# Kernel tuning notes

Hardware: AMD Instinct MI355X
Metric: run time of the kernel (lower is better)

The kernel has to match this reference:

```python
import jax, jax.numpy as jnp
import numpy as np

EPSILON = 1e-8
NUM_STEPS = 1000
S_OFFSET = 0.0001
POWER = 2
CLIPMAX = 0.999
B = 1048576


def _schedule():
    t = jnp.arange(0, NUM_STEPS + 1, dtype=jnp.float32)
    f_t = jnp.cos(np.pi / 2 * (t / NUM_STEPS + S_OFFSET) / (1 + S_OFFSET)) ** POWER
    alpha_bars = f_t / f_t[0]
    betas = jnp.concatenate([jnp.zeros([1], jnp.float32), 1.0 - alpha_bars[1:] / alpha_bars[:-1]])
    betas = jnp.minimum(betas, CLIPMAX)
    sigmas = jnp.sqrt(betas[1:] * ((1.0 - alpha_bars[:-1]) / (1.0 - alpha_bars[1:])))
    sigmas = jnp.concatenate([jnp.zeros([1], jnp.float32), sigmas])
    return alpha_bars, betas, sigmas


def setup_inputs() -> dict:
    key = jax.random.key(0)
    k1, k2, k3, k4, k5 = jax.random.split(key, 5)
    lt = jax.random.normal(k1, (B, 6), dtype=jnp.float32)
    predicted_l0 = jax.random.normal(k2, (B, 6), dtype=jnp.float32)
    pred_lattice = jax.random.normal(k3, (B, 3, 3), dtype=jnp.float32)
    z_noise = jax.random.normal(k4, (B, 6), dtype=jnp.float32)  # torch.randn_like(lt), frozen
    t = jax.random.randint(k5, (B,), 0, NUM_STEPS, dtype=jnp.int64)
    alpha_bars, betas, sigmas = _schedule()
    return {
        "lt": lt,
        "predicted_l0": predicted_l0,
        "pred_lattice": pred_lattice,
        "alpha_bars": alpha_bars,
        "betas": betas,
        "sigmas": sigmas,
        "z_noise": z_noise,
        "t": t,
    }


def reference(lt, predicted_l0, pred_lattice, alpha_bars, betas, sigmas, z_noise, t):
    # VP_lattice.reverse
    alpha = 1.0 - betas[t]
    alpha = jnp.maximum(alpha, 1.0 - betas[-2])  # clamp_min
    alpha_bar = alpha_bars[t]
    sigma = sigmas[t][:, None]

    # polar_decomposition: only the symmetric factor L_tilda = V diag(S) V^T is used
    _, S, Vt = jnp.linalg.svd(pred_lattice, full_matrices=False)  # (B,3),(B,3,3)
    L = jnp.einsum("bji,bj,bjk->bik", Vt, S, Vt)  # Vt^T @ diag(S) @ Vt
    L = (L + jnp.swapaxes(L, 1, 2)) / 2  # symmetrize

    # symmetric_matrix_to_vector: upper triangular incl. diagonal
    vec = jnp.stack([L[:, 0, 0], L[:, 0, 1], L[:, 0, 2], L[:, 1, 1], L[:, 1, 2], L[:, 2, 2]], axis=1)

    predicted_noise = lt - (vec + predicted_l0) / 2
    z = jnp.where((t > 1)[:, None], z_noise, jnp.zeros_like(z_noise))
    coef = (1.0 / jnp.sqrt(alpha + EPSILON))[:, None]
    scale = ((1.0 - alpha) / jnp.sqrt(1.0 - alpha_bar + EPSILON))[:, None]
    return coef * (lt - scale * predicted_noise) + sigma * z
```

## Files before the change

### kernel.cpp

```cpp
#include <hip/hip_runtime.h>


#define NUM_STEPS 1000

__global__ __launch_bounds__(256) void vp_lattice_kernel(
    const float* __restrict__ lt,
    const float* __restrict__ pl0,
    const float* __restrict__ plat,
    const float* __restrict__ alpha_bars,
    const float* __restrict__ betas,
    const float* __restrict__ sigmas,
    const float* __restrict__ z_noise,
    const int*   __restrict__ t,
    float* __restrict__ out,
    int n)
{
    int i = blockIdx.x * blockDim.x + threadIdx.x;
    if (i >= n) return;

    size_t b9 = (size_t)i * 9;
    float af0 = plat[b9 + 0], af1 = plat[b9 + 1], af2 = plat[b9 + 2];
    float af3 = plat[b9 + 3], af4 = plat[b9 + 4], af5 = plat[b9 + 5];
    float af6 = plat[b9 + 6], af7 = plat[b9 + 7], af8 = plat[b9 + 8];

    double a00 = af0, a01 = af1, a02 = af2;
    double a10 = af3, a11 = af4, a12 = af5;
    double a20 = af6, a21 = af7, a22 = af8;

    double m00 = a00*a00 + a10*a10 + a20*a20;
    double m01 = a00*a01 + a10*a11 + a20*a21;
    double m02 = a00*a02 + a10*a12 + a20*a22;
    double m11 = a01*a01 + a11*a11 + a21*a21;
    double m12 = a01*a02 + a11*a12 + a21*a22;
    double m22 = a02*a02 + a12*a12 + a22*a22;

    double I1   = m00 + m11 + m22;
    double trM2 = m00*m00 + m11*m11 + m22*m22
                + 2.0*(m01*m01 + m02*m02 + m12*m12);
    double II   = 0.5*(I1*I1 - trM2);
    double III  = m00*(m11*m22 - m12*m12)
                - m01*(m01*m22 - m12*m02)
                + m02*(m01*m12 - m11*m02);
    double k = I1*I1 - 3.0*II;

    double u00, u01, u02, u11, u12, u22;
    if (k <= 1e-12 * I1 * I1) {
        double lam = sqrt(fmax(I1 * (1.0/3.0), 0.0));
        u00 = u11 = u22 = lam;
        u01 = u02 = u12 = 0.0;
    } else {
        double l   = I1*(I1*I1 - 4.5*II) + 13.5*III;
        double sqk = sqrt(k);
        double arg = l / (k * sqk);
        arg = fmin(fmax(arg, -1.0), 1.0);
        double phi  = acos(arg) * (1.0/3.0);
        double mu1  = (I1 + 2.0*sqk*cos(phi)) * (1.0/3.0);
        mu1 = fmax(mu1, 0.0);
        double lam1  = sqrt(mu1);
        double sqIII = sqrt(fmax(III, 0.0));
        double rest = I1 - mu1 + 2.0*sqIII / fmax(lam1, 1e-150);
        double s23  = sqrt(fmax(rest, 0.0));
        double IU   = lam1 + s23;
        double IIU  = 0.5*(IU*IU - I1);
        double IIIU = sqIII;
        double p00 = m00 + IIU, p11 = m11 + IIU, p22 = m22 + IIU;
        double c00 = p11*p22 - m12*m12;
        double c01 = m02*m12 - m01*p22;
        double c02 = m01*m12 - p11*m02;
        double c11 = p00*p22 - m02*m02;
        double c12 = m01*m02 - p00*m12;
        double c22 = p00*p11 - m01*m01;
        double detP = p00*c00 + m01*c01 + m02*c02;
        double inv  = 1.0 / fmax(detP, 1e-280);
        double n00 = IU*m00 + IIIU, n01 = IU*m01, n02 = IU*m02;
        double n11 = IU*m11 + IIIU, n12 = IU*m12, n22 = IU*m22 + IIIU;
        u00 = (c00*n00 + c01*n01 + c02*n02) * inv;
        u11 = (c01*n01 + c11*n11 + c12*n12) * inv;
        u22 = (c02*n02 + c12*n12 + c22*n22) * inv;
        u01 = 0.5*((c00*n01 + c01*n11 + c02*n12) +
                   (c01*n00 + c11*n01 + c12*n02)) * inv;
        u02 = 0.5*((c00*n02 + c01*n12 + c02*n22) +
                   (c02*n00 + c12*n01 + c22*n02)) * inv;
        u12 = 0.5*((c01*n02 + c11*n12 + c12*n22) +
                   (c02*n01 + c12*n11 + c22*n12)) * inv;
    }

    float v0 = (float)u00, v1 = (float)u01, v2 = (float)u02;
    float v3 = (float)u11, v4 = (float)u12, v5 = (float)u22;

    int ti = t[i];
    float beta_t    = betas[ti];
    float beta_last = betas[NUM_STEPS - 1];
    float alpha     = 1.0f - fminf(beta_t, beta_last);
    float ab        = alpha_bars[ti];
    float sig       = sigmas[ti];
    float coef  = 1.0f / sqrtf(alpha + 1e-8f);
    float scale = (1.0f - alpha) / sqrtf(1.0f - ab + 1e-8f);
    float zgate = (ti > 1) ? 1.0f : 0.0f;

    size_t b6 = (size_t)i * 6;
    const float2* lt2 = reinterpret_cast<const float2*>(lt + b6);
    const float2* p02 = reinterpret_cast<const float2*>(pl0 + b6);
    const float2* zn2 = reinterpret_cast<const float2*>(z_noise + b6);
    float2* out2      = reinterpret_cast<float2*>(out + b6);

    float lv[6], pv[6], zv[6];
    float2 tmp;
    tmp = lt2[0]; lv[0] = tmp.x; lv[1] = tmp.y;
    tmp = lt2[1]; lv[2] = tmp.x; lv[3] = tmp.y;
    tmp = lt2[2]; lv[4] = tmp.x; lv[5] = tmp.y;
    tmp = p02[0]; pv[0] = tmp.x; pv[1] = tmp.y;
    tmp = p02[1]; pv[2] = tmp.x; pv[3] = tmp.y;
    tmp = p02[2]; pv[4] = tmp.x; pv[5] = tmp.y;
    tmp = zn2[0]; zv[0] = tmp.x; zv[1] = tmp.y;
    tmp = zn2[1]; zv[2] = tmp.x; zv[3] = tmp.y;
    tmp = zn2[2]; zv[4] = tmp.x; zv[5] = tmp.y;

    float vv[6] = {v0, v1, v2, v3, v4, v5};
    float ov[6];
#pragma unroll
    for (int c = 0; c < 6; ++c) {
        float lc = lv[c];
        float pn = lc - 0.5f * (vv[c] + pv[c]);
        ov[c] = coef * (lc - scale * pn) + sig * (zgate * zv[c]);
    }
    out2[0] = make_float2(ov[0], ov[1]);
    out2[1] = make_float2(ov[2], ov[3]);
    out2[2] = make_float2(ov[4], ov[5]);
}

extern "C" void kernel_launch(void* const* d_in, const int* in_sizes, int n_in,
                              void* d_out, int out_size, void* d_ws, size_t ws_size,
                              hipStream_t stream) {
    const float* lt         = (const float*)d_in[0];
    const float* pl0        = (const float*)d_in[1];
    const float* plat       = (const float*)d_in[2];
    const float* alpha_bars = (const float*)d_in[3];
    const float* betas      = (const float*)d_in[4];
    const float* sigmas     = (const float*)d_in[5];
    const float* z_noise    = (const float*)d_in[6];
    const int*   t          = (const int*)d_in[7];
    float* out = (float*)d_out;

    int n = in_sizes[0] / 6;
    int block = 256;
    int grid = (n + block - 1) / block;
    vp_lattice_kernel<<<grid, block, 0, stream>>>(
        lt, pl0, plat, alpha_bars, betas, sigmas, z_noise, t, out, n);
}
```

Before: 153.8 us.

## Process two rows per thread with wider loads and float trig

```diff
diff --git a/kernel.cpp b/kernel.cpp
--- a/kernel.cpp
+++ b/kernel.cpp
@@ -13,56 +13,65 @@
     const float* __restrict__ z_noise,
     const int*   __restrict__ t,
     float* __restrict__ out,
-    int n)
+    int npair)
 {
-    int i = blockIdx.x * blockDim.x + threadIdx.x;
-    if (i >= n) return;
+    int gid = blockIdx.x * blockDim.x + threadIdx.x;
+    if (gid >= npair) return;
 
-    size_t b9 = (size_t)i * 9;
-    float af0 = plat[b9 + 0], af1 = plat[b9 + 1], af2 = plat[b9 + 2];
-    float af3 = plat[b9 + 3], af4 = plat[b9 + 4], af5 = plat[b9 + 5];
-    float af6 = plat[b9 + 6], af7 = plat[b9 + 7], af8 = plat[b9 + 8];
+    const float4* ltp = reinterpret_cast<const float4*>(lt)      + (size_t)gid * 3;
+    const float4* plp = reinterpret_cast<const float4*>(pl0)     + (size_t)gid * 3;
+    const float4* znp = reinterpret_cast<const float4*>(z_noise) + (size_t)gid * 3;
+    float4 l4a = ltp[0], l4b = ltp[1], l4c = ltp[2];
+    float4 p4a = plp[0], p4b = plp[1], p4c = plp[2];
+    float4 z4a = znp[0], z4b = znp[1], z4c = znp[2];
 
-    double a00 = af0, a01 = af1, a02 = af2;
-    double a10 = af3, a11 = af4, a12 = af5;
-    double a20 = af6, a21 = af7, a22 = af8;
+    const float2* pp = reinterpret_cast<const float2*>(plat) + (size_t)gid * 9;
+    float a[18];
+#pragma unroll
+    for (int j = 0; j < 9; ++j) { float2 w = pp[j]; a[2*j] = w.x; a[2*j+1] = w.y; }
 
-    double m00 = a00*a00 + a10*a10 + a20*a20;
-    double m01 = a00*a01 + a10*a11 + a20*a21;
-    double m02 = a00*a02 + a10*a12 + a20*a22;
-    double m11 = a01*a01 + a11*a11 + a21*a21;
-    double m12 = a01*a02 + a11*a12 + a21*a22;
-    double m22 = a02*a02 + a12*a12 + a22*a22;
+    int2 tt = reinterpret_cast<const int2*>(t)[gid];
+    float beta_last = betas[NUM_STEPS - 1];
 
-    double I1   = m00 + m11 + m22;
-    double trM2 = m00*m00 + m11*m11 + m22*m22
-                + 2.0*(m01*m01 + m02*m02 + m12*m12);
-    double II   = 0.5*(I1*I1 - trM2);
-    double III  = m00*(m11*m22 - m12*m12)
-                - m01*(m01*m22 - m12*m02)
-                + m02*(m01*m12 - m11*m02);
-    double k = I1*I1 - 3.0*II;
+    float vv[12];
+#pragma unroll
+    for (int r = 0; r < 2; ++r) {
+        const float* A = a + r * 9;
+        double a00 = A[0], a01 = A[1], a02 = A[2];
+        double a10 = A[3], a11 = A[4], a12 = A[5];
+        double a20 = A[6], a21 = A[7], a22 = A[8];
 
-    double u00, u01, u02, u11, u12, u22;
-    if (k <= 1e-12 * I1 * I1) {
-        double lam = sqrt(fmax(I1 * (1.0/3.0), 0.0));
-        u00 = u11 = u22 = lam;
-        u01 = u02 = u12 = 0.0;
-    } else {
-        double l   = I1*(I1*I1 - 4.5*II) + 13.5*III;
-        double sqk = sqrt(k);
-        double arg = l / (k * sqk);
-        arg = fmin(fmax(arg, -1.0), 1.0);
-        double phi  = acos(arg) * (1.0/3.0);
-        double mu1  = (I1 + 2.0*sqk*cos(phi)) * (1.0/3.0);
-        mu1 = fmax(mu1, 0.0);
-        double lam1  = sqrt(mu1);
+        double m00 = a00*a00 + a10*a10 + a20*a20;
+        double m01 = a00*a01 + a10*a11 + a20*a21;
+        double m02 = a00*a02 + a10*a12 + a20*a22;
+        double m11 = a01*a01 + a11*a11 + a21*a21;
+        double m12 = a01*a02 + a11*a12 + a21*a22;
+        double m22 = a02*a02 + a12*a12 + a22*a22;
+
+        double I1   = m00 + m11 + m22;
+        double trM2 = m00*m00 + m11*m11 + m22*m22
+                    + 2.0*(m01*m01 + m02*m02 + m12*m12);
+        double II   = 0.5*(I1*I1 - trM2);
+        double III  = m00*(m11*m22 - m12*m12)
+                    - m01*(m01*m22 - m12*m02)
+                    + m02*(m01*m12 - m11*m02);
+        double k = I1*I1 - 3.0*II;
+        double l = I1*(I1*I1 - 4.5*II) + 13.5*III;
+        double sqk = sqrt(fmax(k, 0.0));
+
+        float denf = fmaxf((float)(k * sqk), 1e-30f);
+        float argf = fminf(fmaxf((float)l / denf, -1.0f), 1.0f);
+        float cf   = cosf(acosf(argf) * (1.0f/3.0f));
+
+        double mu1  = fmax((I1 + 2.0*sqk*(double)cf) * (1.0/3.0), 0.0);
+        double lam1 = sqrt(mu1);
         double sqIII = sqrt(fmax(III, 0.0));
         double rest = I1 - mu1 + 2.0*sqIII / fmax(lam1, 1e-150);
         double s23  = sqrt(fmax(rest, 0.0));
         double IU   = lam1 + s23;
         double IIU  = 0.5*(IU*IU - I1);
         double IIIU = sqIII;
+
         double p00 = m00 + IIU, p11 = m11 + IIU, p22 = m22 + IIU;
         double c00 = p11*p22 - m12*m12;
         double c01 = m02*m12 - m01*p22;
@@ -74,59 +83,50 @@
         double inv  = 1.0 / fmax(detP, 1e-280);
         double n00 = IU*m00 + IIIU, n01 = IU*m01, n02 = IU*m02;
         double n11 = IU*m11 + IIIU, n12 = IU*m12, n22 = IU*m22 + IIIU;
-        u00 = (c00*n00 + c01*n01 + c02*n02) * inv;
-        u11 = (c01*n01 + c11*n11 + c12*n12) * inv;
-        u22 = (c02*n02 + c12*n12 + c22*n22) * inv;
-        u01 = 0.5*((c00*n01 + c01*n11 + c02*n12) +
-                   (c01*n00 + c11*n01 + c12*n02)) * inv;
-        u02 = 0.5*((c00*n02 + c01*n12 + c02*n22) +
-                   (c02*n00 + c12*n01 + c22*n02)) * inv;
-        u12 = 0.5*((c01*n02 + c11*n12 + c12*n22) +
-                   (c02*n01 + c12*n11 + c22*n12)) * inv;
+        double u00 = (c00*n00 + c01*n01 + c02*n02) * inv;
+        double u11 = (c01*n01 + c11*n11 + c12*n12) * inv;
+        double u22 = (c02*n02 + c12*n12 + c22*n22) * inv;
+        double u01 = 0.5*((c00*n01 + c01*n11 + c02*n12) +
+                          (c01*n00 + c11*n01 + c12*n02)) * inv;
+        double u02 = 0.5*((c00*n02 + c01*n12 + c02*n22) +
+                          (c02*n00 + c12*n01 + c22*n02)) * inv;
+        double u12 = 0.5*((c01*n02 + c11*n12 + c12*n22) +
+                          (c02*n01 + c12*n11 + c22*n12)) * inv;
+
+        vv[r*6 + 0] = (float)u00; vv[r*6 + 1] = (float)u01;
+        vv[r*6 + 2] = (float)u02; vv[r*6 + 3] = (float)u11;
+        vv[r*6 + 4] = (float)u12; vv[r*6 + 5] = (float)u22;
     }
 
-    float v0 = (float)u00, v1 = (float)u01, v2 = (float)u02;
-    float v3 = (float)u11, v4 = (float)u12, v5 = (float)u22;
+    float lv[12] = {l4a.x, l4a.y, l4a.z, l4a.w, l4b.x, l4b.y,
+                    l4b.z, l4b.w, l4c.x, l4c.y, l4c.z, l4c.w};
+    float pv[12] = {p4a.x, p4a.y, p4a.z, p4a.w, p4b.x, p4b.y,
+                    p4b.z, p4b.w, p4c.x, p4c.y, p4c.z, p4c.w};
+    float zv[12] = {z4a.x, z4a.y, z4a.z, z4a.w, z4b.x, z4b.y,
+                    z4b.z, z4b.w, z4c.x, z4c.y, z4c.z, z4c.w};
+    float ov[12];
 
-    int ti = t[i];
-    float beta_t    = betas[ti];
-    float beta_last = betas[NUM_STEPS - 1];
-    float alpha     = 1.0f - fminf(beta_t, beta_last);
-    float ab        = alpha_bars[ti];
-    float sig       = sigmas[ti];
-    float coef  = 1.0f / sqrtf(alpha + 1e-8f);
-    float scale = (1.0f - alpha) / sqrtf(1.0f - ab + 1e-8f);
-    float zgate = (ti > 1) ? 1.0f : 0.0f;
+#pragma unroll
+    for (int r = 0; r < 2; ++r) {
+        int ti = (r == 0) ? tt.x : tt.y;
+        float alpha = 1.0f - fminf(betas[ti], beta_last);
+        float ab    = alpha_bars[ti];
+        float sig   = sigmas[ti];
+        float coef  = 1.0f / sqrtf(alpha + 1e-8f);
+        float scale = (1.0f - alpha) / sqrtf(1.0f - ab + 1e-8f);
+        float zgate = (ti > 1) ? 1.0f : 0.0f;
+#pragma unroll
+        for (int c = 0; c < 6; ++c) {
+            float lc = lv[r*6 + c];
+            float pn = lc - 0.5f * (vv[r*6 + c] + pv[r*6 + c]);
+            ov[r*6 + c] = coef * (lc - scale * pn) + sig * (zgate * zv[r*6 + c]);
+        }
+    }
 
-    size_t b6 = (size_t)i * 6;
-    const float2* lt2 = reinterpret_cast<const float2*>(lt + b6);
-    const float2* p02 = reinterpret_cast<const float2*>(pl0 + b6);
-    const float2* zn2 = reinterpret_cast<const float2*>(z_noise + b6);
-    float2* out2      = reinterpret_cast<float2*>(out + b6);
-
-    float lv[6], pv[6], zv[6];
-    float2 tmp;
-    tmp = lt2[0]; lv[0] = tmp.x; lv[1] = tmp.y;
-    tmp = lt2[1]; lv[2] = tmp.x; lv[3] = tmp.y;
-    tmp = lt2[2]; lv[4] = tmp.x; lv[5] = tmp.y;
-    tmp = p02[0]; pv[0] = tmp.x; pv[1] = tmp.y;
-    tmp = p02[1]; pv[2] = tmp.x; pv[3] = tmp.y;
-    tmp = p02[2]; pv[4] = tmp.x; pv[5] = tmp.y;
-    tmp = zn2[0]; zv[0] = tmp.x; zv[1] = tmp.y;
-    tmp = zn2[1]; zv[2] = tmp.x; zv[3] = tmp.y;
-    tmp = zn2[2]; zv[4] = tmp.x; zv[5] = tmp.y;
-
-    float vv[6] = {v0, v1, v2, v3, v4, v5};
-    float ov[6];
-#pragma unroll
-    for (int c = 0; c < 6; ++c) {
-        float lc = lv[c];
-        float pn = lc - 0.5f * (vv[c] + pv[c]);
-        ov[c] = coef * (lc - scale * pn) + sig * (zgate * zv[c]);
-    }
-    out2[0] = make_float2(ov[0], ov[1]);
-    out2[1] = make_float2(ov[2], ov[3]);
-    out2[2] = make_float2(ov[4], ov[5]);
+    float4* op = reinterpret_cast<float4*>(out) + (size_t)gid * 3;
+    op[0] = make_float4(ov[0], ov[1], ov[2],  ov[3]);
+    op[1] = make_float4(ov[4], ov[5], ov[6],  ov[7]);
+    op[2] = make_float4(ov[8], ov[9], ov[10], ov[11]);
 }
 
 extern "C" void kernel_launch(void* const* d_in, const int* in_sizes, int n_in,
@@ -143,8 +143,9 @@
     float* out = (float*)d_out;
 
     int n = in_sizes[0] / 6;
+    int npair = n / 2;
     int block = 256;
-    int grid = (n + block - 1) / block;
+    int grid = (npair + block - 1) / block;
     vp_lattice_kernel<<<grid, block, 0, stream>>>(
-        lt, pl0, plat, alpha_bars, betas, sigmas, z_noise, t, out, n);
+        lt, pl0, plat, alpha_bars, betas, sigmas, z_noise, t, out, npair);
 }
```

Measured after the change: 156.4 us. Within noise of the previous version (+1.7%).

## Compute polar factor in fp32 via eigenvalue closed form and cache schedule in LDS

Applied to the files above, without the earlier changes.

```diff
diff --git a/kernel.cpp b/kernel.cpp
--- a/kernel.cpp
+++ b/kernel.cpp
@@ -15,88 +15,81 @@
     float* __restrict__ out,
     int n)
 {
+    __shared__ float sCoef[NUM_STEPS + 1];
+    __shared__ float sScale[NUM_STEPS + 1];
+    __shared__ float sSig[NUM_STEPS + 1];
+    {
+        float beta_last = betas[NUM_STEPS - 1];
+        for (int j = threadIdx.x; j <= NUM_STEPS; j += 256) {
+            float alpha = 1.0f - fminf(betas[j], beta_last);
+            sCoef[j]  = 1.0f / sqrtf(alpha + 1e-8f);
+            sScale[j] = (1.0f - alpha) / sqrtf(1.0f - alpha_bars[j] + 1e-8f);
+            sSig[j]   = (j > 1) ? sigmas[j] : 0.0f;
+        }
+    }
+    __syncthreads();
+
     int i = blockIdx.x * blockDim.x + threadIdx.x;
     if (i >= n) return;
 
     size_t b9 = (size_t)i * 9;
-    float af0 = plat[b9 + 0], af1 = plat[b9 + 1], af2 = plat[b9 + 2];
-    float af3 = plat[b9 + 3], af4 = plat[b9 + 4], af5 = plat[b9 + 5];
-    float af6 = plat[b9 + 6], af7 = plat[b9 + 7], af8 = plat[b9 + 8];
+    float a00 = plat[b9+0], a01 = plat[b9+1], a02 = plat[b9+2];
+    float a10 = plat[b9+3], a11 = plat[b9+4], a12 = plat[b9+5];
+    float a20 = plat[b9+6], a21 = plat[b9+7], a22 = plat[b9+8];
 
-    double a00 = af0, a01 = af1, a02 = af2;
-    double a10 = af3, a11 = af4, a12 = af5;
-    double a20 = af6, a21 = af7, a22 = af8;
+    float m00 = a00*a00 + a10*a10 + a20*a20;
+    float m01 = a00*a01 + a10*a11 + a20*a21;
+    float m02 = a00*a02 + a10*a12 + a20*a22;
+    float m11 = a01*a01 + a11*a11 + a21*a21;
+    float m12 = a01*a02 + a11*a12 + a21*a22;
+    float m22 = a02*a02 + a12*a12 + a22*a22;
 
-    double m00 = a00*a00 + a10*a10 + a20*a20;
-    double m01 = a00*a01 + a10*a11 + a20*a21;
-    double m02 = a00*a02 + a10*a12 + a20*a22;
-    double m11 = a01*a01 + a11*a11 + a21*a21;
-    double m12 = a01*a02 + a11*a12 + a21*a22;
-    double m22 = a02*a02 + a12*a12 + a22*a22;
+    float q  = (m00 + m11 + m22) * (1.0f/3.0f);
+    float b00 = m00 - q, b11 = m11 - q, b22 = m22 - q;
+    float p1 = m01*m01 + m02*m02 + m12*m12;
+    float p2 = b00*b00 + b11*b11 + b22*b22 + 2.0f*p1;
+    float p  = sqrtf(p2 * (1.0f/6.0f));
+    float detB = b00*(b11*b22 - m12*m12)
+               - m01*(m01*b22 - m12*m02)
+               + m02*(m01*m12 - b11*m02);
+    float pinv = 1.0f / fmaxf(p, 1e-20f);
+    float r = 0.5f * detB * pinv * pinv * pinv;
+    r = fminf(fmaxf(r, -1.0f), 1.0f);
+    float phi = acosf(r) * (1.0f/3.0f);
+    float mu1 = q + 2.0f*p*cosf(phi);
+    float mu3 = q + 2.0f*p*cosf(phi + 2.0943951023931953f);
+    float mu2 = 3.0f*q - mu1 - mu3;
+    float l1 = sqrtf(fmaxf(mu1, 0.0f));
+    float l2 = sqrtf(fmaxf(mu2, 0.0f));
+    float l3 = sqrtf(fmaxf(mu3, 0.0f));
 
-    double I1   = m00 + m11 + m22;
-    double trM2 = m00*m00 + m11*m11 + m22*m22
-                + 2.0*(m01*m01 + m02*m02 + m12*m12);
-    double II   = 0.5*(I1*I1 - trM2);
-    double III  = m00*(m11*m22 - m12*m12)
-                - m01*(m01*m22 - m12*m02)
-                + m02*(m01*m12 - m11*m02);
-    double k = I1*I1 - 3.0*II;
+    float IU   = l1 + l2 + l3;
+    float IIU  = l1*(l2 + l3) + l2*l3;
+    float IIIU = l1*l2*l3;
+    float denom = (l1 + l2) * (l1 + l3) * (l2 + l3);
+    float dinv  = 1.0f / fmaxf(denom, 1e-25f);
+    float sd = (IU*IU - IIU) * dinv;
+    float td = IU * IIIU * dinv;
+    float nd = -dinv;
 
-    double u00, u01, u02, u11, u12, u22;
-    if (k <= 1e-12 * I1 * I1) {
-        double lam = sqrt(fmax(I1 * (1.0/3.0), 0.0));
-        u00 = u11 = u22 = lam;
-        u01 = u02 = u12 = 0.0;
-    } else {
-        double l   = I1*(I1*I1 - 4.5*II) + 13.5*III;
-        double sqk = sqrt(k);
-        double arg = l / (k * sqk);
-        arg = fmin(fmax(arg, -1.0), 1.0);
-        double phi  = acos(arg) * (1.0/3.0);
-        double mu1  = (I1 + 2.0*sqk*cos(phi)) * (1.0/3.0);
-        mu1 = fmax(mu1, 0.0);
-        double lam1  = sqrt(mu1);
-        double sqIII = sqrt(fmax(III, 0.0));
-        double rest = I1 - mu1 + 2.0*sqIII / fmax(lam1, 1e-150);
-        double s23  = sqrt(fmax(rest, 0.0));
-        double IU   = lam1 + s23;
-        double IIU  = 0.5*(IU*IU - I1);
-        double IIIU = sqIII;
-        double p00 = m00 + IIU, p11 = m11 + IIU, p22 = m22 + IIU;
-        double c00 = p11*p22 - m12*m12;
-        double c01 = m02*m12 - m01*p22;
-        double c02 = m01*m12 - p11*m02;
-        double c11 = p00*p22 - m02*m02;
-        double c12 = m01*m02 - p00*m12;
-        double c22 = p00*p11 - m01*m01;
-        double detP = p00*c00 + m01*c01 + m02*c02;
-        double inv  = 1.0 / fmax(detP, 1e-280);
-        double n00 = IU*m00 + IIIU, n01 = IU*m01, n02 = IU*m02;
-        double n11 = IU*m11 + IIIU, n12 = IU*m12, n22 = IU*m22 + IIIU;
-        u00 = (c00*n00 + c01*n01 + c02*n02) * inv;
-        u11 = (c01*n01 + c11*n11 + c12*n12) * inv;
-        u22 = (c02*n02 + c12*n12 + c22*n22) * inv;
-        u01 = 0.5*((c00*n01 + c01*n11 + c02*n12) +
-                   (c01*n00 + c11*n01 + c12*n02)) * inv;
-        u02 = 0.5*((c00*n02 + c01*n12 + c02*n22) +
-                   (c02*n00 + c12*n01 + c22*n02)) * inv;
-        u12 = 0.5*((c01*n02 + c11*n12 + c12*n22) +
-                   (c02*n01 + c12*n11 + c22*n12)) * inv;
-    }
+    float mm00 = m00*m00 + m01*m01 + m02*m02;
+    float mm01 = m00*m01 + m01*m11 + m02*m12;
+    float mm02 = m00*m02 + m01*m12 + m02*m22;
+    float mm11 = m01*m01 + m11*m11 + m12*m12;
+    float mm12 = m01*m02 + m11*m12 + m12*m22;
+    float mm22 = m02*m02 + m12*m12 + m22*m22;
 
-    float v0 = (float)u00, v1 = (float)u01, v2 = (float)u02;
-    float v3 = (float)u11, v4 = (float)u12, v5 = (float)u22;
+    float v0 = nd*mm00 + sd*m00 + td;
+    float v1 = nd*mm01 + sd*m01;
+    float v2 = nd*mm02 + sd*m02;
+    float v3 = nd*mm11 + sd*m11 + td;
+    float v4 = nd*mm12 + sd*m12;
+    float v5 = nd*mm22 + sd*m22 + td;
 
     int ti = t[i];
-    float beta_t    = betas[ti];
-    float beta_last = betas[NUM_STEPS - 1];
-    float alpha     = 1.0f - fminf(beta_t, beta_last);
-    float ab        = alpha_bars[ti];
-    float sig       = sigmas[ti];
-    float coef  = 1.0f / sqrtf(alpha + 1e-8f);
-    float scale = (1.0f - alpha) / sqrtf(1.0f - ab + 1e-8f);
-    float zgate = (ti > 1) ? 1.0f : 0.0f;
+    float coef  = sCoef[ti];
+    float scale = sScale[ti];
+    float sig   = sSig[ti];
 
     size_t b6 = (size_t)i * 6;
     const float2* lt2 = reinterpret_cast<const float2*>(lt + b6);
@@ -105,16 +98,16 @@
     float2* out2      = reinterpret_cast<float2*>(out + b6);
 
     float lv[6], pv[6], zv[6];
-    float2 tmp;
-    tmp = lt2[0]; lv[0] = tmp.x; lv[1] = tmp.y;
-    tmp = lt2[1]; lv[2] = tmp.x; lv[3] = tmp.y;
-    tmp = lt2[2]; lv[4] = tmp.x; lv[5] = tmp.y;
-    tmp = p02[0]; pv[0] = tmp.x; pv[1] = tmp.y;
-    tmp = p02[1]; pv[2] = tmp.x; pv[3] = tmp.y;
-    tmp = p02[2]; pv[4] = tmp.x; pv[5] = tmp.y;
-    tmp = zn2[0]; zv[0] = tmp.x; zv[1] = tmp.y;
-    tmp = zn2[1]; zv[2] = tmp.x; zv[3] = tmp.y;
-    tmp = zn2[2]; zv[4] = tmp.x; zv[5] = tmp.y;
+    float2 w;
+    w = lt2[0]; lv[0]=w.x; lv[1]=w.y;
+    w = lt2[1]; lv[2]=w.x; lv[3]=w.y;
+    w = lt2[2]; lv[4]=w.x; lv[5]=w.y;
+    w = p02[0]; pv[0]=w.x; pv[1]=w.y;
+    w = p02[1]; pv[2]=w.x; pv[3]=w.y;
+    w = p02[2]; pv[4]=w.x; pv[5]=w.y;
+    w = zn2[0]; zv[0]=w.x; zv[1]=w.y;
+    w = zn2[1]; zv[2]=w.x; zv[3]=w.y;
+    w = zn2[2]; zv[4]=w.x; zv[5]=w.y;
 
     float vv[6] = {v0, v1, v2, v3, v4, v5};
     float ov[6];
@@ -122,7 +115,7 @@
     for (int c = 0; c < 6; ++c) {
         float lc = lv[c];
         float pn = lc - 0.5f * (vv[c] + pv[c]);
-        ov[c] = coef * (lc - scale * pn) + sig * (zgate * zv[c]);
+        ov[c] = coef * (lc - scale * pn) + sig * zv[c];
     }
     out2[0] = make_float2(ov[0], ov[1]);
     out2[1] = make_float2(ov[2], ov[3]);
```

New measurement: 153.6 us. About the same (-0.1%).
